# Kernel optimization log

Measured on AMD Instinct MI355X. Metric: run time of the kernel, lower is better.

## Reference

```python
import jax, jax.numpy as jnp
import numpy as np

GROUPS = 32
EPS = 1e-6


def group_norm(x, gamma, beta):
    # x: [b, c, h, w], normalize over (c//GROUPS, h, w) within each group
    b, c, h, w = x.shape
    xg = x.reshape(b, GROUPS, c // GROUPS, h, w)
    mu = xg.mean(axis=(2, 3, 4), keepdims=True)
    var = xg.var(axis=(2, 3, 4), keepdims=True)
    xn = ((xg - mu) * jax.lax.rsqrt(var + EPS)).reshape(b, c, h, w)
    return xn * gamma[None, :, None, None] + beta[None, :, None, None]


def conv1x1(x, W, b):
    # 1x1 conv == channel GEMM. W: [out_c, in_c]
    return jnp.einsum('bchw,oc->bohw', x, W) + b[None, :, None, None]


def setup_inputs() -> dict:
    key = jax.random.key(0)
    ks = jax.random.split(key, 4)
    B, C, H, W = 4, 512, 64, 64
    wscale = 0.02
    return {
        'x': jax.random.normal(ks[0], (B, C, H, W), dtype=jnp.float32),
        'gn_w': jnp.ones((C,), dtype=jnp.float32),
        'gn_b': jnp.zeros((C,), dtype=jnp.float32),
        'q_w': jax.random.normal(ks[1], (C, C), dtype=jnp.float32) * wscale,
        'q_b': jnp.zeros((C,), dtype=jnp.float32),
        'k_w': jax.random.normal(ks[2], (C, C), dtype=jnp.float32) * wscale,
        'k_b': jnp.zeros((C,), dtype=jnp.float32),
        'v_w': jax.random.normal(ks[3], (C, C), dtype=jnp.float32) * wscale,
        'v_b': jnp.zeros((C,), dtype=jnp.float32),
    }


def reference(x, gn_w, gn_b, q_w, q_b, k_w, k_b, v_w, v_b):
    h_ = group_norm(x, gn_w, gn_b)
    q = conv1x1(h_, q_w, q_b)
    k = conv1x1(h_, k_w, k_b)
    v = conv1x1(h_, v_w, v_b)
    b, c, h, w = q.shape
    hw = h * w
    qf = q.reshape(b, c, hw)
    kf = k.reshape(b, c, hw)
    vf = v.reshape(b, c, hw)
    # attn[b, i, j] = sum_c q[b, c, i] * k[b, c, j] / sqrt(c)
    attn = jnp.einsum('bci,bcj->bij', qf, kf) * (c ** -0.5)
    attn = jax.nn.softmax(attn, axis=2)
    # A[b, c, i] = sum_j v[b, c, j] * attn[b, i, j]  (== bmm(v, attn^T))
    A = jnp.einsum('bcj,bij->bci', vf, attn).reshape(b, c, h, w)
    return x + A
```

## Files before the change

### kernel.cpp

```cpp
#include <hip/hip_runtime.h>
#include <hip/hip_bf16.h>

typedef __hip_bfloat16 bf16;
typedef __attribute__((ext_vector_type(8))) short short8;
typedef __attribute__((ext_vector_type(4))) float f32x4;
typedef __attribute__((ext_vector_type(8))) unsigned short u16x8;
typedef __attribute__((ext_vector_type(4))) unsigned short u16x4;

#define HWSZ 4096
#define CH 512
#define BATCH 4
#define NGROUPS 32
#define CPG 16
#define PER ((size_t)CH * HWSZ)

#define GLL16(gp, lp)                                                         \
  __builtin_amdgcn_global_load_lds(                                           \
      (const __attribute__((address_space(1))) void*)(gp),                    \
      (__attribute__((address_space(3))) void*)(lp), 16, 0, 0)

__device__ __forceinline__ float b2f(bf16 v) { return __bfloat162float(v); }
__device__ __forceinline__ bf16 f2b(float v) { return __float2bfloat16(v); }


__global__ void gn_part_kernel(const float* __restrict__ x, float2* __restrict__ gpart) {
  int bg = blockIdx.x >> 3, chunk = blockIdx.x & 7;
  size_t base = (size_t)bg * (CPG * HWSZ) + (size_t)chunk * 8192;
  int tid = threadIdx.x;
  float s = 0.f, ss = 0.f;
  const float4* xp = (const float4*)(x + base);
#pragma unroll
  for (int it = 0; it < 8; ++it) {
    float4 v = xp[tid + it * 256];
    s += v.x + v.y + v.z + v.w;
    ss += v.x * v.x + v.y * v.y + v.z * v.z + v.w * v.w;
  }
  __shared__ float rs[256], rss[256];
  rs[tid] = s; rss[tid] = ss;
  __syncthreads();
  for (int off = 128; off > 0; off >>= 1) {
    if (tid < off) { rs[tid] += rs[tid + off]; rss[tid] += rss[tid + off]; }
    __syncthreads();
  }
  if (tid == 0) gpart[blockIdx.x] = make_float2(rs[0], rss[0]);
}

__global__ void gn_final_kernel(const float2* __restrict__ gpart,
                                const float* __restrict__ gw, const float* __restrict__ gb,
                                float* __restrict__ sca, float* __restrict__ shf) {
  int idx = blockIdx.x * 256 + threadIdx.x;
  int b = idx >> 9, c = idx & 511;
  int bg = b * NGROUPS + (c >> 4);
  float s = 0.f, ss = 0.f;
#pragma unroll
  for (int t = 0; t < 8; ++t) {
    float2 p = gpart[bg * 8 + t];
    s += p.x; ss += p.y;
  }
  const float N = (float)(CPG * HWSZ);
  float mu = s / N;
  float var = ss / N - mu * mu;
  float inv = rsqrtf(var + 1e-6f);
  float a = inv * gw[c];
  sca[idx] = a;
  shf[idx] = gb[c] - mu * a;
}

__global__ void wconv_kernel(const float* __restrict__ qw, const float* __restrict__ kw,
                             const float* __restrict__ vw,
                             bf16* __restrict__ wq, bf16* __restrict__ wk, bf16* __restrict__ wv) {
  int i = blockIdx.x * 256 + threadIdx.x;
  wq[i] = f2b(qw[i]);
  wk[i] = f2b(kw[i]);
  wv[i] = f2b(vw[i]);
}

__global__ void h_apply_kernel(const float* __restrict__ x, const float* __restrict__ sca,
                               const float* __restrict__ shf, bf16* __restrict__ hT, int b0) {
  int p0 = blockIdx.x * 64, c0 = blockIdx.y * 64;
  int b = b0 + blockIdx.z;
  bf16* hTb = hT + (size_t)blockIdx.z * PER;
  __shared__ bf16 lt[64][66];
  int t = threadIdx.x;
  int pp = (t & 15) * 4, ccb = t >> 4;
#pragma unroll
  for (int it = 0; it < 4; ++it) {
    int cc = ccb + it * 16;
    int c = c0 + cc;
    float a = sca[b * CH + c], s = shf[b * CH + c];
    const float4 xv = *(const float4*)(x + ((size_t)(b * CH + c)) * HWSZ + p0 + pp);
    lt[cc][pp] = f2b(a * xv.x + s);
    lt[cc][pp + 1] = f2b(a * xv.y + s);
    lt[cc][pp + 2] = f2b(a * xv.z + s);
    lt[cc][pp + 3] = f2b(a * xv.w + s);
  }
  __syncthreads();
  int cc = (t & 15) * 4;
#pragma unroll
  for (int it = 0; it < 4; ++it) {
    int pr = (t >> 4) + it * 16;
    u16x4 o;
#pragma unroll
    for (int j = 0; j < 4; ++j) o[j] = *(const unsigned short*)&lt[cc + j][pr];
    *(u16x4*)(hTb + (size_t)(p0 + pr) * CH + c0 + cc) = o;
  }
}


__device__ __forceinline__ void mm_step(const bf16* la, const bf16* lb,
                                        f32x4 acc[4][4], int wm, int wn,
                                        int quad, int tm) {
#pragma unroll
  for (int kk = 0; kk < 2; ++kk) {
    const int go = ((kk * 4 + quad) ^ (tm & 7)) * 8;
    short8 aF[4], bF[4];
#pragma unroll
    for (int mt = 0; mt < 4; ++mt) {
      aF[mt] = *(const short8*)(la + (wm + mt * 16 + tm) * 64 + go);
      bF[mt] = *(const short8*)(lb + (wn + mt * 16 + tm) * 64 + go);
    }
#pragma unroll
    for (int mt = 0; mt < 4; ++mt)
#pragma unroll
      for (int nt = 0; nt < 4; ++nt)
        acc[mt][nt] = __builtin_amdgcn_mfma_f32_16x16x32_bf16(aF[mt], bF[nt],
                                                              acc[mt][nt], 0, 0, 0);
  }
}

#define MFMA_VARS()                                   \
  int tid = threadIdx.x;                              \
  int l = tid & 63, w = tid >> 6;                     \
  int quad = l >> 4, tm = l & 15;                     \
  int wm = (w & 1) * 64, wn = (w >> 1) * 64;          \
  int rr = l >> 3;                                    \
  int swz = ((l & 7) ^ rr) * 8;                       \
  bf16* stbase = smem + w * 2048

#define MSTAGE(bufsel, koff)                          \
  do {                                                \
    bf16* _d = stbase + (bufsel) * 16384;             \
    GLL16(sA0 + (koff), _d);                          \
    GLL16(sA1 + (koff), _d + 512);                    \
    GLL16(sA2 + (koff), _d + 1024);                   \
    GLL16(sA3 + (koff), _d + 1536);                   \
    GLL16(sB0 + (koff), _d + 8192);                   \
    GLL16(sB1 + (koff), _d + 8704);                   \
    GLL16(sB2 + (koff), _d + 9216);                   \
    GLL16(sB3 + (koff), _d + 9728);                   \
  } while (0)

#define MKLOOP(NS)                                                       \
  do {                                                                   \
    MSTAGE(0, 0);                                                        \
    for (int _t = 0; _t < (NS); ++_t) {                                  \
      if (_t + 1 < (NS)) {                                               \
        MSTAGE((_t + 1) & 1, (_t + 1) * 64);                             \
        asm volatile("s_waitcnt vmcnt(8)" ::: "memory");                 \
      } else {                                                           \
        asm volatile("s_waitcnt vmcnt(0)" ::: "memory");                 \
      }                                                                  \
      __builtin_amdgcn_s_barrier();                                      \
      mm_step(smem + (_t & 1) * 16384, smem + (_t & 1) * 16384 + 8192,   \
              acc, wm, wn, quad, tm);                                    \
      __builtin_amdgcn_s_barrier();                                      \
    }                                                                    \
  } while (0)

__global__ __launch_bounds__(256) void qkv_mfma(const bf16* __restrict__ hT,
                                                const bf16* __restrict__ wq,
                                                const bf16* __restrict__ wk,
                                                const bf16* __restrict__ wv,
                                                const float* __restrict__ qb,
                                                const float* __restrict__ kb,
                                                const float* __restrict__ vb,
                                                bf16* __restrict__ qT, bf16* __restrict__ kT,
                                                bf16* __restrict__ v) {
  int p0 = blockIdx.x * 128;
  int o0 = blockIdx.y * 128;
  int bz = blockIdx.z / 3, z = blockIdx.z % 3;
  const bf16* W = z == 0 ? wq : (z == 1 ? wk : wv);
  const float* bias = z == 0 ? qb : (z == 1 ? kb : vb);
  const bf16* hTb = hT + (size_t)bz * PER;
  __shared__ __align__(16) bf16 smem[32768];
  MFMA_VARS();
  const bf16* sA0 = hTb + (size_t)(p0 + w * 32 + rr) * CH + swz;
  const bf16* sA1 = sA0 + (size_t)8 * CH;
  const bf16* sA2 = sA0 + (size_t)16 * CH;
  const bf16* sA3 = sA0 + (size_t)24 * CH;
  const bf16* sB0 = W + (size_t)(o0 + w * 32 + rr) * CH + swz;
  const bf16* sB1 = sB0 + (size_t)8 * CH;
  const bf16* sB2 = sB0 + (size_t)16 * CH;
  const bf16* sB3 = sB0 + (size_t)24 * CH;
  f32x4 acc[4][4] = {};
  MKLOOP(CH / 64);
  if (z < 2) {
    bf16* outT = (z == 0 ? qT : kT) + (size_t)bz * PER;
#pragma unroll
    for (int nt = 0; nt < 4; ++nt) {
      int o = o0 + wn + nt * 16 + tm;
      float bv = bias[o];
#pragma unroll
      for (int mt = 0; mt < 4; ++mt)
#pragma unroll
        for (int r = 0; r < 4; ++r) {
          int p = p0 + wm + mt * 16 + quad * 4 + r;
          outT[(size_t)p * CH + o] = f2b(acc[mt][nt][r] + bv);
        }
    }
  } else {
    bf16* vv = v + (size_t)bz * PER;
    bf16* lt = smem;
    for (int chunk = 0; chunk < 2; ++chunk) {
      __syncthreads();
      if (wn == chunk * 64) {
#pragma unroll
        for (int nt = 0; nt < 4; ++nt) {
          int o = o0 + wn + nt * 16 + tm;
          float bv = bias[o];
#pragma unroll
          for (int mt = 0; mt < 4; ++mt)
#pragma unroll
            for (int r = 0; r < 4; ++r)
              lt[(nt * 16 + tm) * 136 + wm + mt * 16 + quad * 4 + r] = f2b(acc[mt][nt][r] + bv);
        }
      }
      __syncthreads();
      int oo = tid >> 2, ppb = (tid & 3) * 32;
      bf16* dst = vv + (size_t)(o0 + chunk * 64 + oo) * HWSZ + p0 + ppb;
      const bf16* src = lt + oo * 136 + ppb;
#pragma unroll
      for (int q4 = 0; q4 < 4; ++q4)
        *(u16x8*)(dst + q4 * 8) = *(const u16x8*)(src + q4 * 8);
    }
  }
}

__global__ __launch_bounds__(256) void s_mfma(const bf16* __restrict__ qT,
                                              const bf16* __restrict__ kT,
                                              bf16* __restrict__ attn,
                                              float* __restrict__ lsum) {
  int j0 = blockIdx.x * 128;
  int il0 = blockIdx.y * 128;
  int bz = blockIdx.z;
  const bf16* qTb = qT + (size_t)bz * PER;
  const bf16* kTb = kT + (size_t)bz * PER;
  bf16* attnb = attn + (size_t)bz * HWSZ * HWSZ;
  float* lsumb = lsum + (size_t)bz * HWSZ;
  __shared__ __align__(16) bf16 smem[32768];
  MFMA_VARS();
  const bf16* sA0 = qTb + (size_t)(il0 + w * 32 + rr) * CH + swz;
  const bf16* sA1 = sA0 + (size_t)8 * CH;
  const bf16* sA2 = sA0 + (size_t)16 * CH;
  const bf16* sA3 = sA0 + (size_t)24 * CH;
  const bf16* sB0 = kTb + (size_t)(j0 + w * 32 + rr) * CH + swz;
  const bf16* sB1 = sB0 + (size_t)8 * CH;
  const bf16* sB2 = sB0 + (size_t)16 * CH;
  const bf16* sB3 = sB0 + (size_t)24 * CH;
  f32x4 acc[4][4] = {};
  MKLOOP(CH / 64);
  const float scale = 0.044194173824159216f;
#pragma unroll
  for (int mt = 0; mt < 4; ++mt)
#pragma unroll
    for (int r = 0; r < 4; ++r) {
      int il = il0 + wm + mt * 16 + quad * 4 + r;
      float rs = 0.f;
#pragma unroll
      for (int nt = 0; nt < 4; ++nt) {
        float p = __expf(acc[mt][nt][r] * scale);
        rs += p;
        attnb[(size_t)il * HWSZ + j0 + wn + nt * 16 + tm] = f2b(p);
      }
      rs += __shfl_xor(rs, 1);
      rs += __shfl_xor(rs, 2);
      rs += __shfl_xor(rs, 4);
      rs += __shfl_xor(rs, 8);
      if (tm == 0) atomicAdd(&lsumb[il], rs);
    }
}

__global__ __launch_bounds__(256) void a_mfma(const bf16* __restrict__ v,
                                              const bf16* __restrict__ attn,
                                              float* __restrict__ acc_out,
                                              int KC, int ksplit) {
  int il0 = blockIdx.x * 128;
  int c00 = blockIdx.y * 128;
  int bz = blockIdx.z / ksplit;
  int kbase = (blockIdx.z % ksplit) * KC;
  const bf16* vb = v + (size_t)bz * PER;
  const bf16* attnb = attn + (size_t)bz * HWSZ * HWSZ;
  float* accb = acc_out + (size_t)bz * CH * HWSZ;
  __shared__ __align__(16) bf16 smem[32768];
  MFMA_VARS();
  const bf16* sA0 = vb + (size_t)(c00 + w * 32 + rr) * HWSZ + kbase + swz;
  const bf16* sA1 = sA0 + (size_t)8 * HWSZ;
  const bf16* sA2 = sA0 + (size_t)16 * HWSZ;
  const bf16* sA3 = sA0 + (size_t)24 * HWSZ;
  const bf16* sB0 = attnb + (size_t)(il0 + w * 32 + rr) * HWSZ + kbase + swz;
  const bf16* sB1 = sB0 + (size_t)8 * HWSZ;
  const bf16* sB2 = sB0 + (size_t)16 * HWSZ;
  const bf16* sB3 = sB0 + (size_t)24 * HWSZ;
  f32x4 acc[4][4] = {};
  MKLOOP(KC / 64);
#pragma unroll
  for (int mt = 0; mt < 4; ++mt)
#pragma unroll
    for (int nt = 0; nt < 4; ++nt)
#pragma unroll
      for (int r = 0; r < 4; ++r) {
        int c = c00 + wm + mt * 16 + quad * 4 + r;
        int il = il0 + wn + nt * 16 + tm;
        atomicAdd(&accb[(size_t)c * HWSZ + il], acc[mt][nt][r]);
      }
}

__global__ void add_kernel(const float* __restrict__ x, const float* __restrict__ acc,
                           const float* __restrict__ lsum, float* __restrict__ out, int b0) {
  int idx = blockIdx.x * 256 + threadIdx.x;
  int b = b0 + blockIdx.y;
  const float* accb = acc + (size_t)blockIdx.y * CH * HWSZ;
  const float* lsumb = lsum + (size_t)blockIdx.y * HWSZ;
  int c = idx >> 10;
  int r4 = (idx & 1023) * 4;
  size_t g = ((size_t)(b * CH + c)) * HWSZ + r4;
  const float4 xv = *(const float4*)(x + g);
  const float4 av = *(const float4*)(accb + (size_t)c * HWSZ + r4);
  const float4 lv = *(const float4*)(lsumb + r4);
  float4 o;
  o.x = xv.x + av.x / lv.x;
  o.y = xv.y + av.y / lv.y;
  o.z = xv.z + av.z / lv.z;
  o.w = xv.w + av.w / lv.w;
  *(float4*)(out + g) = o;
}

extern "C" void kernel_launch(void* const* d_in, const int* in_sizes, int n_in,
                              void* d_out, int out_size, void* d_ws, size_t ws_size,
                              hipStream_t stream) {
  const float* x   = (const float*)d_in[0];
  const float* gnw = (const float*)d_in[1];
  const float* gnb = (const float*)d_in[2];
  const float* qw  = (const float*)d_in[3];
  const float* qb  = (const float*)d_in[4];
  const float* kw  = (const float*)d_in[5];
  const float* kb  = (const float*)d_in[6];
  const float* vw  = (const float*)d_in[7];
  const float* vb  = (const float*)d_in[8];
  float* out = (float*)d_out;

  char* ws = (char*)d_ws;
  float* sca = (float*)ws;
  float* shf = sca + BATCH * CH;
  float2* gpart = (float2*)(ws + 16384);
  const size_t wsz = (size_t)CH * CH;
  bf16* wqb = (bf16*)(ws + 32768);
  bf16* wkb = wqb + wsz;
  bf16* wvb = wkb + wsz;
  char* dyn = (char*)(wvb + wsz);
  size_t base_used = (size_t)(dyn - ws);
  size_t perb = 4 * PER * sizeof(bf16) + (size_t)HWSZ * HWSZ * sizeof(bf16) +
                (size_t)CH * HWSZ * sizeof(float) + (size_t)HWSZ * sizeof(float);
  int nb = (int)(((long long)ws_size - (long long)base_used) / (long long)perb);
  if (nb < 1) nb = 1;
  if (nb > BATCH) nb = BATCH;
  bf16* hT = (bf16*)dyn;
  bf16* qT = hT + (size_t)nb * PER;
  bf16* kT = qT + (size_t)nb * PER;
  bf16* v  = kT + (size_t)nb * PER;
  bf16* attn = v + (size_t)nb * PER;
  float* acc = (float*)(attn + (size_t)nb * HWSZ * HWSZ);
  float* lsum = acc + (size_t)nb * CH * HWSZ;

  gn_part_kernel<<<dim3(BATCH * NGROUPS * 8), 256, 0, stream>>>(x, gpart);
  gn_final_kernel<<<dim3(8), 256, 0, stream>>>(gpart, gnw, gnb, sca, shf);
  wconv_kernel<<<dim3(wsz / 256), 256, 0, stream>>>(qw, kw, vw, wqb, wkb, wvb);
  for (int b0 = 0; b0 < BATCH; b0 += nb) {
    int nbc = BATCH - b0 < nb ? BATCH - b0 : nb;
    h_apply_kernel<<<dim3(HWSZ / 64, CH / 64, nbc), 256, 0, stream>>>(x, sca, shf, hT, b0);
    qkv_mfma<<<dim3(HWSZ / 128, CH / 128, 3 * nbc), 256, 0, stream>>>(hT, wqb, wkb, wvb,
                                                                      qb, kb, vb, qT, kT, v);
    hipMemsetAsync(acc, 0, (size_t)nbc * CH * HWSZ * sizeof(float), stream);
    hipMemsetAsync(lsum, 0, (size_t)nbc * HWSZ * sizeof(float), stream);
    int ksplit = 4 / nbc;
    if (ksplit < 1) ksplit = 1;
    int KC = HWSZ / ksplit;
    s_mfma<<<dim3(HWSZ / 128, HWSZ / 128, nbc), 256, 0, stream>>>(qT, kT, attn, lsum);
    a_mfma<<<dim3(HWSZ / 128, CH / 128, ksplit * nbc), 256, 0, stream>>>(v, attn, acc, KC, ksplit);
    add_kernel<<<dim3((CH * HWSZ) / 1024, nbc), 256, 0, stream>>>(x, acc, lsum, out, b0);
  }
}
```

Before: 358.2 us.

## Loop S kernel over multiple j tiles and fuse attention-V with residual add

The score kernel now has each block handle JL consecutive 128-column tiles. The next tile's Q/K stage is prefetched across tile boundaries, so the same Q rows are reused and the grid shrinks. When two or more batches run together, a new fused A kernel does the full K reduction without split-K. It then applies the softmax normalisation and residual add directly, which removes the accumulator memset, the float atomics/accumulator traffic and the separate add kernel. The cost is fewer blocks in flight for both kernels and less parallelism in the fused path.

After: 319.7 us. -10.7%, faster.

```diff
diff --git a/kernel.cpp b/kernel.cpp
--- a/kernel.cpp
+++ b/kernel.cpp
@@ -13,6 +13,7 @@
 #define NGROUPS 32
 #define CPG 16
 #define PER ((size_t)CH * HWSZ)
+#define JL 4
 
 #define GLL16(gp, lp)                                                         \
   __builtin_amdgcn_global_load_lds(                                           \
@@ -21,7 +22,6 @@
 
 __device__ __forceinline__ float b2f(bf16 v) { return __bfloat162float(v); }
 __device__ __forceinline__ bf16 f2b(float v) { return __float2bfloat16(v); }
-
 
 __global__ void gn_part_kernel(const float* __restrict__ x, float2* __restrict__ gpart) {
   int bg = blockIdx.x >> 3, chunk = blockIdx.x & 7;
@@ -236,11 +236,24 @@
   }
 }
 
+#define SSTAGE(bufsel, koff, jof)                      \
+  do {                                                 \
+    bf16* _d = stbase + (bufsel) * 16384;              \
+    GLL16(sA0 + (koff), _d);                           \
+    GLL16(sA1 + (koff), _d + 512);                     \
+    GLL16(sA2 + (koff), _d + 1024);                    \
+    GLL16(sA3 + (koff), _d + 1536);                    \
+    GLL16(sB0 + (jof) + (koff), _d + 8192);            \
+    GLL16(sB1 + (jof) + (koff), _d + 8704);            \
+    GLL16(sB2 + (jof) + (koff), _d + 9216);            \
+    GLL16(sB3 + (jof) + (koff), _d + 9728);            \
+  } while (0)
+
 __global__ __launch_bounds__(256) void s_mfma(const bf16* __restrict__ qT,
                                               const bf16* __restrict__ kT,
                                               bf16* __restrict__ attn,
                                               float* __restrict__ lsum) {
-  int j0 = blockIdx.x * 128;
+  int j0base = blockIdx.x * (128 * JL);
   int il0 = blockIdx.y * 128;
   int bz = blockIdx.z;
   const bf16* qTb = qT + (size_t)bz * PER;
@@ -253,31 +266,91 @@
   const bf16* sA1 = sA0 + (size_t)8 * CH;
   const bf16* sA2 = sA0 + (size_t)16 * CH;
   const bf16* sA3 = sA0 + (size_t)24 * CH;
-  const bf16* sB0 = kTb + (size_t)(j0 + w * 32 + rr) * CH + swz;
+  const bf16* sB0 = kTb + (size_t)(j0base + w * 32 + rr) * CH + swz;
   const bf16* sB1 = sB0 + (size_t)8 * CH;
   const bf16* sB2 = sB0 + (size_t)16 * CH;
   const bf16* sB3 = sB0 + (size_t)24 * CH;
+  const float scale = 0.044194173824159216f;
+  SSTAGE(0, 0, 0);
+  for (int jj = 0; jj < JL; ++jj) {
+    const size_t jof = (size_t)jj * 128 * CH;
+    const size_t jofn = (size_t)(jj + 1) * 128 * CH;
+    f32x4 acc[4][4] = {};
+    for (int _t = 0; _t < 8; ++_t) {
+      if (_t + 1 < 8) {
+        SSTAGE((_t + 1) & 1, (_t + 1) * 64, jof);
+        asm volatile("s_waitcnt vmcnt(8)" ::: "memory");
+      } else if (jj + 1 < JL) {
+        SSTAGE(0, 0, jofn);
+        asm volatile("s_waitcnt vmcnt(8)" ::: "memory");
+      } else {
+        asm volatile("s_waitcnt vmcnt(0)" ::: "memory");
+      }
+      __builtin_amdgcn_s_barrier();
+      mm_step(smem + (_t & 1) * 16384, smem + (_t & 1) * 16384 + 8192,
+              acc, wm, wn, quad, tm);
+      __builtin_amdgcn_s_barrier();
+    }
+    int j0 = j0base + jj * 128;
+#pragma unroll
+    for (int mt = 0; mt < 4; ++mt)
+#pragma unroll
+      for (int r = 0; r < 4; ++r) {
+        int il = il0 + wm + mt * 16 + quad * 4 + r;
+        float rs = 0.f;
+#pragma unroll
+        for (int nt = 0; nt < 4; ++nt) {
+          float p = __expf(acc[mt][nt][r] * scale);
+          rs += p;
+          attnb[(size_t)il * HWSZ + j0 + wn + nt * 16 + tm] = f2b(p);
+        }
+        rs += __shfl_xor(rs, 1);
+        rs += __shfl_xor(rs, 2);
+        rs += __shfl_xor(rs, 4);
+        rs += __shfl_xor(rs, 8);
+        if (tm == 0) atomicAdd(&lsumb[il], rs);
+      }
+  }
+}
+
+__global__ __launch_bounds__(256) void a_mfma_fused(const bf16* __restrict__ v,
+                                                    const bf16* __restrict__ attn,
+                                                    const float* __restrict__ x,
+                                                    const float* __restrict__ lsum,
+                                                    float* __restrict__ out, int b0) {
+  int il0 = blockIdx.x * 128;
+  int c00 = blockIdx.y * 128;
+  int bz = blockIdx.z;
+  const bf16* vb = v + (size_t)bz * PER;
+  const bf16* attnb = attn + (size_t)bz * HWSZ * HWSZ;
+  const float* lsumb = lsum + (size_t)bz * HWSZ;
+  const float* xb = x + (size_t)(b0 + bz) * CH * HWSZ;
+  float* outb = out + (size_t)(b0 + bz) * CH * HWSZ;
+  __shared__ __align__(16) bf16 smem[32768];
+  MFMA_VARS();
+  const bf16* sA0 = vb + (size_t)(c00 + w * 32 + rr) * HWSZ + swz;
+  const bf16* sA1 = sA0 + (size_t)8 * HWSZ;
+  const bf16* sA2 = sA0 + (size_t)16 * HWSZ;
+  const bf16* sA3 = sA0 + (size_t)24 * HWSZ;
+  const bf16* sB0 = attnb + (size_t)(il0 + w * 32 + rr) * HWSZ + swz;
+  const bf16* sB1 = sB0 + (size_t)8 * HWSZ;
+  const bf16* sB2 = sB0 + (size_t)16 * HWSZ;
+  const bf16* sB3 = sB0 + (size_t)24 * HWSZ;
   f32x4 acc[4][4] = {};
-  MKLOOP(CH / 64);
-  const float scale = 0.044194173824159216f;
-#pragma unroll
-  for (int mt = 0; mt < 4; ++mt)
-#pragma unroll
-    for (int r = 0; r < 4; ++r) {
-      int il = il0 + wm + mt * 16 + quad * 4 + r;
-      float rs = 0.f;
-#pragma unroll
-      for (int nt = 0; nt < 4; ++nt) {
-        float p = __expf(acc[mt][nt][r] * scale);
-        rs += p;
-        attnb[(size_t)il * HWSZ + j0 + wn + nt * 16 + tm] = f2b(p);
+  MKLOOP(HWSZ / 64);
+#pragma unroll
+  for (int nt = 0; nt < 4; ++nt) {
+    int il = il0 + wn + nt * 16 + tm;
+    float rl = 1.0f / lsumb[il];
+#pragma unroll
+    for (int mt = 0; mt < 4; ++mt)
+#pragma unroll
+      for (int r = 0; r < 4; ++r) {
+        int c = c00 + wm + mt * 16 + quad * 4 + r;
+        size_t g = (size_t)c * HWSZ + il;
+        outb[g] = xb[g] + acc[mt][nt][r] * rl;
       }
-      rs += __shfl_xor(rs, 1);
-      rs += __shfl_xor(rs, 2);
-      rs += __shfl_xor(rs, 4);
-      rs += __shfl_xor(rs, 8);
-      if (tm == 0) atomicAdd(&lsumb[il], rs);
-    }
+  }
 }
 
 __global__ __launch_bounds__(256) void a_mfma(const bf16* __restrict__ v,
@@ -380,13 +453,18 @@
     h_apply_kernel<<<dim3(HWSZ / 64, CH / 64, nbc), 256, 0, stream>>>(x, sca, shf, hT, b0);
     qkv_mfma<<<dim3(HWSZ / 128, CH / 128, 3 * nbc), 256, 0, stream>>>(hT, wqb, wkb, wvb,
                                                                       qb, kb, vb, qT, kT, v);
-    hipMemsetAsync(acc, 0, (size_t)nbc * CH * HWSZ * sizeof(float), stream);
     hipMemsetAsync(lsum, 0, (size_t)nbc * HWSZ * sizeof(float), stream);
-    int ksplit = 4 / nbc;
-    if (ksplit < 1) ksplit = 1;
-    int KC = HWSZ / ksplit;
-    s_mfma<<<dim3(HWSZ / 128, HWSZ / 128, nbc), 256, 0, stream>>>(qT, kT, attn, lsum);
-    a_mfma<<<dim3(HWSZ / 128, CH / 128, ksplit * nbc), 256, 0, stream>>>(v, attn, acc, KC, ksplit);
-    add_kernel<<<dim3((CH * HWSZ) / 1024, nbc), 256, 0, stream>>>(x, acc, lsum, out, b0);
-  }
-}
+    s_mfma<<<dim3(HWSZ / (128 * JL), HWSZ / 128, nbc), 256, 0, stream>>>(qT, kT, attn, lsum);
+    if (nbc >= 2) {
+      a_mfma_fused<<<dim3(HWSZ / 128, CH / 128, nbc), 256, 0, stream>>>(v, attn, x, lsum,
+                                                                        out, b0);
+    } else {
+      hipMemsetAsync(acc, 0, (size_t)nbc * CH * HWSZ * sizeof(float), stream);
+      int ksplit = 4;
+      int KC = HWSZ / ksplit;
+      a_mfma<<<dim3(HWSZ / 128, CH / 128, ksplit * nbc), 256, 0, stream>>>(v, attn, acc, KC,
+                                                                           ksplit);
+      add_kernel<<<dim3((CH * HWSZ) / 1024, nbc), 256, 0, stream>>>(x, acc, lsum, out, b0);
+    }
+  }
+}
```
